# Kernel optimization log

Hardware: AMD Instinct MI355X
Metric: run time of the kernel (lower is better)

The kernel has to match this reference:

```python
import jax, jax.numpy as jnp
import numpy as np

B, L, D, H = 2, 2048, 1024, 16
DK = D // H
EPS = 1e-6


def setup_inputs() -> dict:
    key = jax.random.key(0)
    ks = jax.random.split(key, 8)
    s = 0.02
    return {
        "key": jax.random.normal(ks[0], (B, L, D), jnp.float32),
        "value": jax.random.normal(ks[1], (B, L, D), jnp.float32),
        "query": jax.random.normal(ks[2], (B, L, D), jnp.float32),
        "mask": jax.random.randint(ks[3], (B, L, L), 0, 2).astype(bool),
        "W_k": jax.random.normal(ks[4], (D, D), jnp.float32) * s,
        "W_v": jax.random.normal(ks[5], (D, D), jnp.float32) * s,
        "W_q": jax.random.normal(ks[6], (D, D), jnp.float32) * s,
        "ln_g": jnp.ones((D,), jnp.float32),
        "ln_b": jnp.zeros((D,), jnp.float32),
    }


def _mha(key, value, query, mask, W_k, W_v, W_q, ln_g, ln_b):
    b, l, d = key.shape
    # projections (bias=False), split into heads: [b, h, l, dk]
    def proj(x, W):
        return (x @ W).reshape(b, -1, H, DK).transpose(0, 2, 1, 3)
    k_up, v_up, q_up = proj(key, W_k), proj(value, W_v), proj(query, W_q)
    # scores [b, h, q, k]
    scores = jnp.einsum("bhqd,bhkd->bhqk", q_up, k_up) / jnp.sqrt(jnp.asarray(DK, scores_dtype(q_up)))
    scores = jnp.where(mask[:, None, :, :], -1e9, scores)
    attn = jax.nn.softmax(scores, axis=-1)  # dropout = identity (eval mode)
    out = jnp.einsum("bhqk,bhkd->bhqd", attn, v_up)
    out = out.transpose(0, 2, 1, 3).reshape(b, -1, d)
    res = out + query  # res_dropout = identity
    mu = jnp.mean(res, axis=-1, keepdims=True)
    var = jnp.var(res, axis=-1, keepdims=True)
    normed = (res - mu) * jax.lax.rsqrt(var + EPS) * ln_g + ln_b
    return normed, attn.reshape(b * H, attn.shape[2], attn.shape[3])


def scores_dtype(x):
    return x.dtype


def reference(key, value, query, mask, W_k, W_v, W_q, ln_g, ln_b):
    return _mha(key, value, query, mask, W_k, W_v, W_q, ln_g, ln_b)
```

## Files before the change

### kernel.cpp

```cpp
#include <hip/hip_runtime.h>
#include <math.h>

#define BATCH 2
#define SEQ   2048
#define DMODEL 1024
#define NHEAD 16
#define DK    64
#define EPS   1e-6f

typedef unsigned short ushort_t;
typedef __attribute__((ext_vector_type(8))) __bf16 bf16x8;
typedef __attribute__((ext_vector_type(4))) float f32x4;
typedef __attribute__((ext_vector_type(4))) unsigned int uivec4;

union B8U { uivec4 u; bf16x8 v; };

__device__ __forceinline__ ushort_t f2b(float x) {
    union { float f; unsigned int u; } c; c.f = x;
    unsigned int r = (c.u + 0x7fffu + ((c.u >> 16) & 1u)) >> 16;
    return (ushort_t)r;
}
__device__ __forceinline__ float b2f(ushort_t b) {
    union { unsigned int u; float f; } c; c.u = ((unsigned int)b) << 16;
    return c.f;
}
__device__ __forceinline__ bf16x8 ld_frag_lds(const ushort_t* p) {
    B8U t; t.u = *reinterpret_cast<const uivec4*>(p); return t.v;
}
__device__ __forceinline__ bf16x8 ld_frag_glb(const ushort_t* p) {
    B8U t; t.u = *reinterpret_cast<const uivec4*>(p); return t.v;
}
__device__ __forceinline__ void gload_lds16(const ushort_t* g, ushort_t* l) {
    __builtin_amdgcn_global_load_lds(
        (const __attribute__((address_space(1))) unsigned int*)g,
        (__attribute__((address_space(3))) unsigned int*)l,
        16, 0, 0);
}
#define MFMA16(a, b, c) __builtin_amdgcn_mfma_f32_16x16x32_bf16((a), (b), (c), 0, 0, 0)

__global__ __launch_bounds__(256) void mask_to_bits(const int* __restrict__ mask,
                                                    unsigned int* __restrict__ bits) {
    const size_t widx = (size_t)blockIdx.x * 256 + threadIdx.x;
    const int4* src = reinterpret_cast<const int4*>(mask + widx * 32);
    unsigned int wv = 0;
    #pragma unroll
    for (int i = 0; i < 8; ++i) {
        int4 v = src[i];
        wv |= (v.x ? 1u : 0u) << (i * 4 + 0);
        wv |= (v.y ? 1u : 0u) << (i * 4 + 1);
        wv |= (v.z ? 1u : 0u) << (i * 4 + 2);
        wv |= (v.w ? 1u : 0u) << (i * 4 + 3);
    }
    bits[widx] = wv;
}

__global__ __launch_bounds__(256) void cvt_bf16x3(const float* __restrict__ X0,
                                                  const float* __restrict__ X1,
                                                  const float* __restrict__ X2,
                                                  ushort_t* __restrict__ Y0,
                                                  ushort_t* __restrict__ Y1,
                                                  ushort_t* __restrict__ Y2) {
    const int z = blockIdx.y;
    const float* X = (z == 0) ? X0 : (z == 1) ? X1 : X2;
    ushort_t*    Y = (z == 0) ? Y0 : (z == 1) ? Y1 : Y2;
    const size_t i = ((size_t)blockIdx.x * 256 + threadIdx.x) * 8;
    float4 a = *reinterpret_cast<const float4*>(X + i);
    float4 b = *reinterpret_cast<const float4*>(X + i + 4);
    ushort_t o[8];
    o[0] = f2b(a.x); o[1] = f2b(a.y); o[2] = f2b(a.z); o[3] = f2b(a.w);
    o[4] = f2b(b.x); o[5] = f2b(b.y); o[6] = f2b(b.z); o[7] = f2b(b.w);
    *reinterpret_cast<uivec4*>(Y + i) = *reinterpret_cast<const uivec4*>(o);
}

__global__ __launch_bounds__(256) void transpose_w3(const float* __restrict__ W0,
                                                    const float* __restrict__ W1,
                                                    const float* __restrict__ W2,
                                                    ushort_t* __restrict__ T0,
                                                    ushort_t* __restrict__ T1,
                                                    ushort_t* __restrict__ T2) {
    __shared__ ushort_t tile[64][68];
    const int z = blockIdx.z;
    const float* W = (z == 0) ? W0 : (z == 1) ? W1 : W2;
    ushort_t*    T = (z == 0) ? T0 : (z == 1) ? T1 : T2;
    const int k0 = blockIdx.x * 64;
    const int n0 = blockIdx.y * 64;
    const int t = threadIdx.x;
    {
        const int r = t >> 2, c0 = (t & 3) * 16;
        const float* src = W + (size_t)(k0 + r) * DMODEL + n0 + c0;
        #pragma unroll
        for (int i = 0; i < 16; ++i) tile[r][c0 + i] = f2b(src[i]);
    }
    __syncthreads();
    {
        const int c = t >> 2, r0 = (t & 3) * 16;
        ushort_t* dst = T + (size_t)(n0 + c) * DMODEL + k0 + r0;
        #pragma unroll
        for (int i = 0; i < 16; ++i) dst[i] = tile[r0 + i][c];
    }
}

__global__ __launch_bounds__(256) void gemm_proj3(const ushort_t* __restrict__ Xb0,
                                                  const ushort_t* __restrict__ Xb1,
                                                  const ushort_t* __restrict__ Xb2,
                                                  const ushort_t* __restrict__ Wt0,
                                                  const ushort_t* __restrict__ Wt1,
                                                  const ushort_t* __restrict__ Wt2,
                                                  ushort_t* __restrict__ Y0,
                                                  ushort_t* __restrict__ Y1,
                                                  ushort_t* __restrict__ Y2) {
    __shared__ __align__(16) ushort_t As[128 * 32];
    __shared__ __align__(16) ushort_t Bs[128 * 32];
    const int z = blockIdx.z;
    const ushort_t* Xb = (z == 0) ? Xb0 : (z == 1) ? Xb1 : Xb2;
    const ushort_t* Wt = (z == 0) ? Wt0 : (z == 1) ? Wt1 : Wt2;
    ushort_t*       Y  = (z == 0) ? Y0  : (z == 1) ? Y1  : Y2;

    const int t = threadIdx.x;
    const int bm = blockIdx.y * 128;
    const int bn = blockIdx.x * 128;
    const int w = t >> 6, lane = t & 63;
    const int ln16 = lane & 15, quad = lane >> 4;
    const int wr = w >> 1, wc = w & 1;

    const int srow = lane >> 2;
    const int selem = (lane & 3) * 8;

    f32x4 acc[4][4] = {};

    for (int k0 = 0; k0 < DMODEL; k0 += 32) {
        #pragma unroll
        for (int j = 0; j < 2; ++j) {
            const int g = w * 2 + j;
            const int m = g * 16 + srow;
            gload_lds16(Xb + (size_t)(bm + m) * DMODEL + k0 + selem, &As[g * 512]);
            gload_lds16(Wt + (size_t)(bn + m) * DMODEL + k0 + selem, &Bs[g * 512]);
        }
        __syncthreads();
        bf16x8 af[4], bfr[4];
        #pragma unroll
        for (int rt = 0; rt < 4; ++rt)
            af[rt] = ld_frag_lds(&As[(wr * 64 + rt * 16 + ln16) * 32 + quad * 8]);
        #pragma unroll
        for (int ct = 0; ct < 4; ++ct)
            bfr[ct] = ld_frag_lds(&Bs[(wc * 64 + ct * 16 + ln16) * 32 + quad * 8]);
        __builtin_amdgcn_s_setprio(1);
        #pragma unroll
        for (int rt = 0; rt < 4; ++rt)
            #pragma unroll
            for (int ct = 0; ct < 4; ++ct)
                acc[rt][ct] = MFMA16(af[rt], bfr[ct], acc[rt][ct]);
        __builtin_amdgcn_s_setprio(0);
        __syncthreads();
    }
    #pragma unroll
    for (int rt = 0; rt < 4; ++rt) {
        #pragma unroll
        for (int ct = 0; ct < 4; ++ct) {
            #pragma unroll
            for (int r = 0; r < 4; ++r) {
                int row = bm + wr * 64 + rt * 16 + quad * 4 + r;
                int col = bn + wc * 64 + ct * 16 + ln16;
                Y[(size_t)row * DMODEL + col] = f2b(acc[rt][ct][r]);
            }
        }
    }
}

__global__ __launch_bounds__(256) void transpose_v(const ushort_t* __restrict__ v_up,
                                                   ushort_t* __restrict__ v_t) {
    __shared__ ushort_t tile[64][68];
    const int t = threadIdx.x;
    const int s0 = blockIdx.x * 64;
    const int bh = blockIdx.y;
    const int b = bh >> 4, h = bh & 15;
    {
        const int r = t >> 2, c0 = (t & 3) * 16;
        const ushort_t* src = v_up + ((size_t)b * SEQ + s0 + r) * DMODEL + h * DK + c0;
        #pragma unroll
        for (int i = 0; i < 16; ++i) tile[r][c0 + i] = src[i];
    }
    __syncthreads();
    {
        const int c = t >> 2, r0 = (t & 3) * 16;
        ushort_t* dst = v_t + ((size_t)bh * DK + c) * SEQ + s0 + r0;
        #pragma unroll
        for (int i = 0; i < 16; ++i) dst[i] = tile[r0 + i][c];
    }
}

#define PST 264
__global__ __launch_bounds__(512, 4) void attn_fused(const ushort_t* __restrict__ q_up,
                                                     const ushort_t* __restrict__ k_up,
                                                     const ushort_t* __restrict__ v_t,
                                                     const unsigned int* __restrict__ mbits,
                                                     float* __restrict__ attn,
                                                     float* __restrict__ o_ws) {
    __shared__ __align__(16) ushort_t Pb[32 * PST];
    __shared__ float psum[8][32];
    __shared__ float inv_s[32];

    const int t = threadIdx.x;
    const int w = t >> 6, lane = t & 63;
    const int ln16 = lane & 15, quad = lane >> 4;
    const int q0 = blockIdx.x * 32;
    const int bh = blockIdx.y;
    const int b = bh >> 4, h = bh & 15;

    bf16x8 aq[2][2];
    #pragma unroll
    for (int rt = 0; rt < 2; ++rt)
        #pragma unroll
        for (int ks = 0; ks < 2; ++ks)
            aq[rt][ks] = ld_frag_glb(
                &q_up[((size_t)b * SEQ + q0 + rt * 16 + ln16) * DMODEL + h * DK + ks * 32 + quad * 8]);

    const unsigned int* mrow = mbits + ((size_t)b * SEQ + q0) * (SEQ / 32);
    const ushort_t* kbase = &k_up[(size_t)b * SEQ * DMODEL + h * DK + quad * 8];

    float rs[2][4] = {};
    for (int i = 0; i < 16; ++i) {
        const int kt = (i * 8 + w) * 16;
        bf16x8 bk0 = ld_frag_glb(kbase + (size_t)(kt + ln16) * DMODEL);
        bf16x8 bk1 = ld_frag_glb(kbase + (size_t)(kt + ln16) * DMODEL + 32);
        const int wi = kt >> 5;
        const int bsh = (kt & 16) + ln16;
        #pragma unroll
        for (int rt = 0; rt < 2; ++rt) {
            f32x4 c = {0.f, 0.f, 0.f, 0.f};
            __builtin_amdgcn_s_setprio(1);
            c = MFMA16(aq[rt][0], bk0, c);
            c = MFMA16(aq[rt][1], bk1, c);
            __builtin_amdgcn_s_setprio(0);
            #pragma unroll
            for (int r = 0; r < 4; ++r) {
                const int row = rt * 16 + quad * 4 + r;
                const unsigned int mw = mrow[(size_t)row * (SEQ / 32) + wi];
                const float p = ((mw >> bsh) & 1u) ? 0.f : __expf(c[r] * 0.125f);
                rs[rt][r] += p;
            }
        }
    }
    #pragma unroll
    for (int rt = 0; rt < 2; ++rt)
        #pragma unroll
        for (int r = 0; r < 4; ++r) {
            float v = rs[rt][r];
            v += __shfl_xor(v, 1);
            v += __shfl_xor(v, 2);
            v += __shfl_xor(v, 4);
            v += __shfl_xor(v, 8);
            rs[rt][r] = v;
        }
    if (ln16 == 0) {
        #pragma unroll
        for (int rt = 0; rt < 2; ++rt)
            #pragma unroll
            for (int r = 0; r < 4; ++r)
                psum[w][rt * 16 + quad * 4 + r] = rs[rt][r];
    }
    __syncthreads();
    if (t < 32) {
        float s = 0.f;
        #pragma unroll
        for (int j = 0; j < 8; ++j) s += psum[j][t];
        inv_s[t] = 1.f / s;
    }
    __syncthreads();
    float invr[2][4];
    #pragma unroll
    for (int rt = 0; rt < 2; ++rt)
        #pragma unroll
        for (int r = 0; r < 4; ++r)
            invr[rt][r] = inv_s[rt * 16 + quad * 4 + r];

    const int prt = w >> 2, pct = w & 3;
    f32x4 acc = {0.f, 0.f, 0.f, 0.f};
    const ushort_t* vbase = &v_t[((size_t)bh * DK + pct * 16 + ln16) * SEQ + quad * 8];
    float* abase = attn + ((size_t)bh * SEQ + q0) * SEQ;
    const ushort_t* prow = &Pb[(prt * 16 + ln16) * PST + quad * 8];

    for (int kb = 0; kb < SEQ; kb += 256) {
        #pragma unroll
        for (int tl = 0; tl < 2; ++tl) {
            const int kt = kb + (w * 2 + tl) * 16;
            bf16x8 bk0 = ld_frag_glb(kbase + (size_t)(kt + ln16) * DMODEL);
            bf16x8 bk1 = ld_frag_glb(kbase + (size_t)(kt + ln16) * DMODEL + 32);
            const int wi = kt >> 5;
            const int bsh = (kt & 16) + ln16;
            #pragma unroll
            for (int rt = 0; rt < 2; ++rt) {
                f32x4 c = {0.f, 0.f, 0.f, 0.f};
                __builtin_amdgcn_s_setprio(1);
                c = MFMA16(aq[rt][0], bk0, c);
                c = MFMA16(aq[rt][1], bk1, c);
                __builtin_amdgcn_s_setprio(0);
                #pragma unroll
                for (int r = 0; r < 4; ++r) {
                    const int row = rt * 16 + quad * 4 + r;
                    const unsigned int mw = mrow[(size_t)row * (SEQ / 32) + wi];
                    const float p = ((mw >> bsh) & 1u) ? 0.f : __expf(c[r] * 0.125f);
                    const float pn = p * invr[rt][r];
                    __builtin_nontemporal_store(pn, &abase[(size_t)row * SEQ + kt + ln16]);
                    Pb[row * PST + (kt - kb) + ln16] = f2b(pn);
                }
            }
        }
        __syncthreads();
        __builtin_amdgcn_s_setprio(1);
        #pragma unroll
        for (int k0 = 0; k0 < 256; k0 += 32) {
            bf16x8 a  = ld_frag_lds(prow + k0);
            bf16x8 vb = ld_frag_glb(vbase + kb + k0);
            acc = MFMA16(a, vb, acc);
        }
        __builtin_amdgcn_s_setprio(0);
        __syncthreads();
    }
    #pragma unroll
    for (int r = 0; r < 4; ++r) {
        const int row = q0 + prt * 16 + quad * 4 + r;
        const int col = h * DK + pct * 16 + ln16;
        o_ws[((size_t)b * SEQ + row) * DMODEL + col] = acc[r];
    }
}

__global__ __launch_bounds__(256) void ln_kernel(const float* __restrict__ O,
                                                 const float* __restrict__ Qin,
                                                 const float* __restrict__ g,
                                                 const float* __restrict__ bt,
                                                 float* __restrict__ out) {
    __shared__ float sm[256];
    const int tid = threadIdx.x;
    const size_t base = (size_t)blockIdx.x * DMODEL;
    float v[4];
    float s = 0.f, s2 = 0.f;
    #pragma unroll
    for (int i = 0; i < 4; ++i) {
        int d = tid + i * 256;
        float x = O[base + d] + Qin[base + d];
        v[i] = x;
        s += x;
        s2 += x * x;
    }
    sm[tid] = s; __syncthreads();
    for (int st = 128; st > 0; st >>= 1) {
        if (tid < st) sm[tid] += sm[tid + st];
        __syncthreads();
    }
    s = sm[0]; __syncthreads();
    sm[tid] = s2; __syncthreads();
    for (int st = 128; st > 0; st >>= 1) {
        if (tid < st) sm[tid] += sm[tid + st];
        __syncthreads();
    }
    s2 = sm[0];
    const float mu = s * (1.0f / DMODEL);
    const float var = s2 * (1.0f / DMODEL) - mu * mu;
    const float r = rsqrtf(var + EPS);
    #pragma unroll
    for (int i = 0; i < 4; ++i) {
        int d = tid + i * 256;
        out[base + d] = (v[i] - mu) * r * g[d] + bt[d];
    }
}

extern "C" void kernel_launch(void* const* d_in, const int* in_sizes, int n_in,
                              void* d_out, int out_size, void* d_ws, size_t ws_size,
                              hipStream_t stream) {
    const float* key   = (const float*)d_in[0];
    const float* value = (const float*)d_in[1];
    const float* query = (const float*)d_in[2];
    const int*   mask  = (const int*)  d_in[3];
    const float* W_k   = (const float*)d_in[4];
    const float* W_v   = (const float*)d_in[5];
    const float* W_q   = (const float*)d_in[6];
    const float* ln_g  = (const float*)d_in[7];
    const float* ln_b  = (const float*)d_in[8];

    float* out      = (float*)d_out;
    float* attn_out = out + (size_t)BATCH * SEQ * DMODEL;

    const size_t NPROJ = (size_t)BATCH * SEQ * DMODEL;
    const size_t NW    = (size_t)DMODEL * DMODEL;
    ushort_t* k_up = (ushort_t*)d_ws;
    ushort_t* v_up = k_up + NPROJ;
    ushort_t* q_up = v_up + NPROJ;
    ushort_t* v_t  = q_up + NPROJ;
    ushort_t* kb   = v_t + NPROJ;
    ushort_t* vb   = kb + NPROJ;
    ushort_t* qb   = vb + NPROJ;
    ushort_t* wtk  = qb + NPROJ;
    ushort_t* wtv  = wtk + NW;
    ushort_t* wtq  = wtv + NW;
    float*    o_ws = (float*)(wtq + NW);
    unsigned int* mbits = (unsigned int*)(o_ws + NPROJ);

    const int nwords = BATCH * SEQ * (SEQ / 32);
    mask_to_bits<<<nwords / 256, 256, 0, stream>>>(mask, mbits);

    dim3 gcvt((unsigned)(NPROJ / (256 * 8)), 3);
    cvt_bf16x3<<<gcvt, 256, 0, stream>>>(key, value, query, kb, vb, qb);

    dim3 gtw(DMODEL / 64, DMODEL / 64, 3);
    transpose_w3<<<gtw, 256, 0, stream>>>(W_k, W_v, W_q, wtk, wtv, wtq);

    dim3 gproj(DMODEL / 128, (BATCH * SEQ) / 128, 3);
    gemm_proj3<<<gproj, 256, 0, stream>>>(kb, vb, qb, wtk, wtv, wtq, k_up, v_up, q_up);

    dim3 gtr(SEQ / 64, BATCH * NHEAD);
    transpose_v<<<gtr, 256, 0, stream>>>(v_up, v_t);

    dim3 gat(SEQ / 32, BATCH * NHEAD);
    attn_fused<<<gat, 512, 0, stream>>>(q_up, k_up, v_t, mbits, attn_out, o_ws);

    ln_kernel<<<BATCH * SEQ, 256, 0, stream>>>(o_ws, query, ln_g, ln_b, out);
}
```

Baseline: 931.7 us.

## Cache unnormalized probabilities in registers and write attn rows vectorized from LDS

The first pass now packs the unnormalized exp scores into 64 registers as bf16 pairs. The second pass reuses them instead of reloading K, recomputing the QK^T MFMAs and the mask exps, and only normalizes and writes them to LDS. The attention matrix is then written to global with coalesced 16-byte nontemporal stores read back from the bf16 LDS tile, replacing scattered scalar stores. The attn output now carries bf16 rounding, applied twice, which adds error to a float32 output, and the 64-register array raises register pressure. The s_setprio calls are also removed.

```diff
diff --git a/kernel.cpp b/kernel.cpp
--- a/kernel.cpp
+++ b/kernel.cpp
@@ -144,13 +144,11 @@
         #pragma unroll
         for (int ct = 0; ct < 4; ++ct)
             bfr[ct] = ld_frag_lds(&Bs[(wc * 64 + ct * 16 + ln16) * 32 + quad * 8]);
-        __builtin_amdgcn_s_setprio(1);
         #pragma unroll
         for (int rt = 0; rt < 4; ++rt)
             #pragma unroll
             for (int ct = 0; ct < 4; ++ct)
                 acc[rt][ct] = MFMA16(af[rt], bfr[ct], acc[rt][ct]);
-        __builtin_amdgcn_s_setprio(0);
         __syncthreads();
     }
     #pragma unroll
@@ -218,27 +216,30 @@
     const unsigned int* mrow = mbits + ((size_t)b * SEQ + q0) * (SEQ / 32);
     const ushort_t* kbase = &k_up[(size_t)b * SEQ * DMODEL + h * DK + quad * 8];
 
+    unsigned int pp[64];
     float rs[2][4] = {};
+    const int bsh = ((w & 1) * 16) + ln16;
+    #pragma unroll
     for (int i = 0; i < 16; ++i) {
-        const int kt = (i * 8 + w) * 16;
+        const int kt = i * 128 + w * 16;
         bf16x8 bk0 = ld_frag_glb(kbase + (size_t)(kt + ln16) * DMODEL);
         bf16x8 bk1 = ld_frag_glb(kbase + (size_t)(kt + ln16) * DMODEL + 32);
-        const int wi = kt >> 5;
-        const int bsh = (kt & 16) + ln16;
+        const int wi = i * 4 + (w >> 1);
         #pragma unroll
         for (int rt = 0; rt < 2; ++rt) {
             f32x4 c = {0.f, 0.f, 0.f, 0.f};
-            __builtin_amdgcn_s_setprio(1);
             c = MFMA16(aq[rt][0], bk0, c);
             c = MFMA16(aq[rt][1], bk1, c);
-            __builtin_amdgcn_s_setprio(0);
+            float pv[4];
             #pragma unroll
             for (int r = 0; r < 4; ++r) {
                 const int row = rt * 16 + quad * 4 + r;
                 const unsigned int mw = mrow[(size_t)row * (SEQ / 32) + wi];
-                const float p = ((mw >> bsh) & 1u) ? 0.f : __expf(c[r] * 0.125f);
-                rs[rt][r] += p;
+                pv[r] = ((mw >> bsh) & 1u) ? 0.f : __expf(c[r] * 0.125f);
+                rs[rt][r] += pv[r];
             }
+            pp[i * 4 + rt * 2 + 0] = (unsigned int)f2b(pv[0]) | ((unsigned int)f2b(pv[1]) << 16);
+            pp[i * 4 + rt * 2 + 1] = (unsigned int)f2b(pv[2]) | ((unsigned int)f2b(pv[3]) << 16);
         }
     }
     #pragma unroll
@@ -279,42 +280,51 @@
     const ushort_t* vbase = &v_t[((size_t)bh * DK + pct * 16 + ln16) * SEQ + quad * 8];
     float* abase = attn + ((size_t)bh * SEQ + q0) * SEQ;
     const ushort_t* prow = &Pb[(prt * 16 + ln16) * PST + quad * 8];
-
-    for (int kb = 0; kb < SEQ; kb += 256) {
+    const int arow = t >> 4;
+    const int acol0 = (t & 15) * 16;
+
+    #pragma unroll
+    for (int j = 0; j < 8; ++j) {
+        const int kb = j * 256;
         #pragma unroll
         for (int tl = 0; tl < 2; ++tl) {
-            const int kt = kb + (w * 2 + tl) * 16;
-            bf16x8 bk0 = ld_frag_glb(kbase + (size_t)(kt + ln16) * DMODEL);
-            bf16x8 bk1 = ld_frag_glb(kbase + (size_t)(kt + ln16) * DMODEL + 32);
-            const int wi = kt >> 5;
-            const int bsh = (kt & 16) + ln16;
+            const int i = j * 2 + tl;
+            const int rcol = tl * 128 + w * 16 + ln16;
             #pragma unroll
             for (int rt = 0; rt < 2; ++rt) {
-                f32x4 c = {0.f, 0.f, 0.f, 0.f};
-                __builtin_amdgcn_s_setprio(1);
-                c = MFMA16(aq[rt][0], bk0, c);
-                c = MFMA16(aq[rt][1], bk1, c);
-                __builtin_amdgcn_s_setprio(0);
                 #pragma unroll
-                for (int r = 0; r < 4; ++r) {
-                    const int row = rt * 16 + quad * 4 + r;
-                    const unsigned int mw = mrow[(size_t)row * (SEQ / 32) + wi];
-                    const float p = ((mw >> bsh) & 1u) ? 0.f : __expf(c[r] * 0.125f);
-                    const float pn = p * invr[rt][r];
-                    __builtin_nontemporal_store(pn, &abase[(size_t)row * SEQ + kt + ln16]);
-                    Pb[row * PST + (kt - kb) + ln16] = f2b(pn);
+                for (int hlf = 0; hlf < 2; ++hlf) {
+                    const unsigned int pk = pp[i * 4 + rt * 2 + hlf];
+                    #pragma unroll
+                    for (int rr = 0; rr < 2; ++rr) {
+                        const int r = hlf * 2 + rr;
+                        const int row = rt * 16 + quad * 4 + r;
+                        const float p = b2f((ushort_t)((pk >> (rr * 16)) & 0xffffu));
+                        Pb[row * PST + rcol] = f2b(p * invr[rt][r]);
+                    }
                 }
             }
         }
         __syncthreads();
-        __builtin_amdgcn_s_setprio(1);
+        {
+            const ushort_t* src = &Pb[arow * PST + acol0];
+            float* dst = abase + (size_t)arow * SEQ + kb + acol0;
+            #pragma unroll
+            for (int v4 = 0; v4 < 4; ++v4) {
+                f32x4 o;
+                o[0] = b2f(src[v4 * 4 + 0]);
+                o[1] = b2f(src[v4 * 4 + 1]);
+                o[2] = b2f(src[v4 * 4 + 2]);
+                o[3] = b2f(src[v4 * 4 + 3]);
+                __builtin_nontemporal_store(o, reinterpret_cast<f32x4*>(dst + v4 * 4));
+            }
+        }
         #pragma unroll
         for (int k0 = 0; k0 < 256; k0 += 32) {
             bf16x8 a  = ld_frag_lds(prow + k0);
             bf16x8 vb = ld_frag_glb(vbase + kb + k0);
             acc = MFMA16(a, vb, acc);
         }
-        __builtin_amdgcn_s_setprio(0);
         __syncthreads();
     }
     #pragma unroll
```

After: 1.572 ms. 68.7% more time.

## Coalesce attention-probability stores via LDS, remap block order, raise occupancy

Applied to the files above, without the earlier changes.

The attention kernel no longer writes the fp32 probability matrix with scattered per-element stores from MFMA fragments. It now reads the bf16 P tile back from shared memory after the barrier and writes contiguous 16-float rows per thread with vectorized nontemporal stores. It also remaps the block index so consecutive blocks cover different heads, raises the min-blocks hint from 4 to 6, and removes the setprio calls in both kernels. The cost is that the stored attn values are rounded to bf16 before being widened back to fp32, which lowers output precision, and the higher occupancy hint may force register spills.

```diff
diff --git a/kernel.cpp b/kernel.cpp
--- a/kernel.cpp
+++ b/kernel.cpp
@@ -35,6 +35,14 @@
         (const __attribute__((address_space(1))) unsigned int*)g,
         (__attribute__((address_space(3))) unsigned int*)l,
         16, 0, 0);
+}
+__device__ __forceinline__ f32x4 unpk2(unsigned int w0, unsigned int w1) {
+    f32x4 o;
+    o[0] = b2f((ushort_t)(w0 & 0xffffu));
+    o[1] = b2f((ushort_t)(w0 >> 16));
+    o[2] = b2f((ushort_t)(w1 & 0xffffu));
+    o[3] = b2f((ushort_t)(w1 >> 16));
+    return o;
 }
 #define MFMA16(a, b, c) __builtin_amdgcn_mfma_f32_16x16x32_bf16((a), (b), (c), 0, 0, 0)
 
@@ -144,13 +152,11 @@
         #pragma unroll
         for (int ct = 0; ct < 4; ++ct)
             bfr[ct] = ld_frag_lds(&Bs[(wc * 64 + ct * 16 + ln16) * 32 + quad * 8]);
-        __builtin_amdgcn_s_setprio(1);
         #pragma unroll
         for (int rt = 0; rt < 4; ++rt)
             #pragma unroll
             for (int ct = 0; ct < 4; ++ct)
                 acc[rt][ct] = MFMA16(af[rt], bfr[ct], acc[rt][ct]);
-        __builtin_amdgcn_s_setprio(0);
         __syncthreads();
     }
     #pragma unroll
@@ -190,7 +196,7 @@
 }
 
 #define PST 264
-__global__ __launch_bounds__(512, 4) void attn_fused(const ushort_t* __restrict__ q_up,
+__global__ __launch_bounds__(512, 6) void attn_fused(const ushort_t* __restrict__ q_up,
                                                      const ushort_t* __restrict__ k_up,
                                                      const ushort_t* __restrict__ v_t,
                                                      const unsigned int* __restrict__ mbits,
@@ -203,8 +209,11 @@
     const int t = threadIdx.x;
     const int w = t >> 6, lane = t & 63;
     const int ln16 = lane & 15, quad = lane >> 4;
-    const int q0 = blockIdx.x * 32;
-    const int bh = blockIdx.y;
+
+    const int orig = blockIdx.x + gridDim.x * blockIdx.y;
+    const int j8 = orig >> 3;
+    const int bh = (orig & 7) * 4 + (j8 >> 6);
+    const int q0 = (j8 & 63) * 32;
     const int b = bh >> 4, h = bh & 15;
 
     bf16x8 aq[2][2];
@@ -228,10 +237,8 @@
         #pragma unroll
         for (int rt = 0; rt < 2; ++rt) {
             f32x4 c = {0.f, 0.f, 0.f, 0.f};
-            __builtin_amdgcn_s_setprio(1);
             c = MFMA16(aq[rt][0], bk0, c);
             c = MFMA16(aq[rt][1], bk1, c);
-            __builtin_amdgcn_s_setprio(0);
             #pragma unroll
             for (int r = 0; r < 4; ++r) {
                 const int row = rt * 16 + quad * 4 + r;
@@ -279,6 +286,8 @@
     const ushort_t* vbase = &v_t[((size_t)bh * DK + pct * 16 + ln16) * SEQ + quad * 8];
     float* abase = attn + ((size_t)bh * SEQ + q0) * SEQ;
     const ushort_t* prow = &Pb[(prt * 16 + ln16) * PST + quad * 8];
+    const int arow = t >> 4;
+    const int acol0 = (t & 15) * 16;
 
     for (int kb = 0; kb < SEQ; kb += 256) {
         #pragma unroll
@@ -291,30 +300,34 @@
             #pragma unroll
             for (int rt = 0; rt < 2; ++rt) {
                 f32x4 c = {0.f, 0.f, 0.f, 0.f};
-                __builtin_amdgcn_s_setprio(1);
                 c = MFMA16(aq[rt][0], bk0, c);
                 c = MFMA16(aq[rt][1], bk1, c);
-                __builtin_amdgcn_s_setprio(0);
                 #pragma unroll
                 for (int r = 0; r < 4; ++r) {
                     const int row = rt * 16 + quad * 4 + r;
                     const unsigned int mw = mrow[(size_t)row * (SEQ / 32) + wi];
                     const float p = ((mw >> bsh) & 1u) ? 0.f : __expf(c[r] * 0.125f);
-                    const float pn = p * invr[rt][r];
-                    __builtin_nontemporal_store(pn, &abase[(size_t)row * SEQ + kt + ln16]);
-                    Pb[row * PST + (kt - kb) + ln16] = f2b(pn);
+                    Pb[row * PST + (kt - kb) + ln16] = f2b(p * invr[rt][r]);
                 }
             }
         }
         __syncthreads();
-        __builtin_amdgcn_s_setprio(1);
+        {
+            const ushort_t* srcp = &Pb[arow * PST + acol0];
+            float* dst = abase + (size_t)arow * SEQ + kb + acol0;
+            const uivec4 pa = *reinterpret_cast<const uivec4*>(srcp);
+            const uivec4 pb2 = *reinterpret_cast<const uivec4*>(srcp + 8);
+            __builtin_nontemporal_store(unpk2(pa[0], pa[1]), reinterpret_cast<f32x4*>(dst));
+            __builtin_nontemporal_store(unpk2(pa[2], pa[3]), reinterpret_cast<f32x4*>(dst + 4));
+            __builtin_nontemporal_store(unpk2(pb2[0], pb2[1]), reinterpret_cast<f32x4*>(dst + 8));
+            __builtin_nontemporal_store(unpk2(pb2[2], pb2[3]), reinterpret_cast<f32x4*>(dst + 12));
+        }
         #pragma unroll
         for (int k0 = 0; k0 < 256; k0 += 32) {
             bf16x8 a  = ld_frag_lds(prow + k0);
             bf16x8 vb = ld_frag_glb(vbase + kb + k0);
             acc = MFMA16(a, vb, acc);
         }
-        __builtin_amdgcn_s_setprio(0);
         __syncthreads();
     }
     #pragma unroll
```

Result: slower. 1.635 ms (+75.5%).
